# Optimization experiments

Hardware: AMD Instinct MI355X
Metric: run time of the kernel (lower is better)

## Reference

```python
import jax, jax.numpy as jnp
import numpy as np

B, N = 256, 20000

def setup_inputs() -> dict:
    key = jax.random.key(0)
    k1, k2 = jax.random.split(key)
    x_in = jax.random.normal(k1, (B, 1, N, 4), dtype=jnp.float32)
    weights = jax.random.uniform(k2, (B, N), dtype=jnp.float32)
    return {"x_in": x_in, "weights": weights}

def reference(x_in, weights):
    # weighted_8points: x_in [B,1,N,4] -> e_hat [B,9]
    b, _, n, _ = x_in.shape
    xx = x_in[:, 0, :, :]                      # [B,N,4] = (x1, y1, x2, y2)
    x1, y1, x2, y2 = xx[..., 0], xx[..., 1], xx[..., 2], xx[..., 3]
    ones = jnp.ones_like(x1)
    # Epipolar design matrix rows: [x2*x1, x2*y1, x2, y2*x1, y2*y1, y2, x1, y1, 1]
    X = jnp.stack([x2 * x1, x2 * y1, x2,
                   y2 * x1, y2 * y1, y2,
                   x1, y1, ones], axis=-1)      # [B,N,9]
    wX = weights[:, :, None] * X                # [B,N,9]
    XwX = jnp.einsum('bni,bnj->bij', X, wX)     # [B,9,9] symmetric
    # batch_symeig: eigenvectors ascending by eigenvalue; smallest -> column 0
    _, v = jnp.linalg.eigh(XwX)                 # [B,9,9]
    e_hat = v[:, :, 0]                          # [B,9]
    e_hat = e_hat / jnp.linalg.norm(e_hat, axis=1, keepdims=True)
    return e_hat
```

## Files before the change

### kernel.cpp

```cpp
#include <hip/hip_runtime.h>
#include <math.h>

#define BATCH 256
#define NPTS  20000
#define NCHUNK 4
#define PERCH (NPTS / NCHUNK)

__global__ __launch_bounds__(256) void gram_kernel(
    const float4* __restrict__ x, const float* __restrict__ w,
    double* __restrict__ partial)
{
    int b = blockIdx.x;
    int chunk = blockIdx.y;
    int tid = threadIdx.x;

    float acc[45];
#pragma unroll
    for (int k = 0; k < 45; ++k) acc[k] = 0.0f;

    const float4* xb = x + (size_t)b * NPTS;
    const float*  wb = w + (size_t)b * NPTS;
    int base = chunk * PERCH;
    for (int n = base + tid; n < base + PERCH; n += 256) {
        float4 v = xb[n];
        float wt = wb[n];
        float X[9];
        X[0] = v.z * v.x; X[1] = v.z * v.y; X[2] = v.z;
        X[3] = v.w * v.x; X[4] = v.w * v.y; X[5] = v.w;
        X[6] = v.x;       X[7] = v.y;       X[8] = 1.0f;
        int idx = 0;
#pragma unroll
        for (int j = 0; j < 9; ++j) {
            float wXj = wt * X[j];
#pragma unroll
            for (int i = j; i < 9; ++i) {
                acc[idx] += X[i] * wXj;
                ++idx;
            }
        }
    }

#pragma unroll
    for (int k = 0; k < 45; ++k) {
        float v = acc[k];
        for (int off = 32; off > 0; off >>= 1)
            v += __shfl_down(v, off, 64);
        acc[k] = v;
    }
    __shared__ float red[4][45];
    int lane = tid & 63, wv = tid >> 6;
    if (lane == 0) {
#pragma unroll
        for (int k = 0; k < 45; ++k) red[wv][k] = acc[k];
    }
    __syncthreads();
    if (tid < 45) {
        double s = (double)red[0][tid] + (double)red[1][tid]
                 + (double)red[2][tid] + (double)red[3][tid];
        partial[((size_t)b * NCHUNK + chunk) * 45 + tid] = s;
    }
}


__device__ __forceinline__ float f_sign(float a, float b) {
    return (b >= 0.0f) ? fabsf(a) : -fabsf(a);
}

__device__ __forceinline__ float slapy2(float xx, float yy) {
    float xa = fabsf(xx), ya = fabsf(yy);
    float w_ = fmaxf(xa, ya), z_ = fminf(xa, ya);
    if (z_ == 0.0f) return w_;
    float t = z_ / w_;
    return w_ * sqrtf(1.0f + t * t);
}

__device__ __forceinline__ void slartg(float f, float g, float* cs, float* sn, float* r) {
    if (g == 0.0f) { *cs = 1.0f; *sn = 0.0f; *r = f; }
    else if (f == 0.0f) { *cs = 0.0f; *sn = (g >= 0.0f) ? 1.0f : -1.0f; *r = fabsf(g); }
    else {
        float dd = sqrtf(f * f + g * g);
        *cs = fabsf(f) / dd;
        *r  = f_sign(dd, f);
        *sn = g / (*r);
    }
}

__device__ void slaev2(float a, float b, float c_, float* rt1, float* rt2,
                       float* cs1, float* sn1) {
    float sm = a + c_;
    float df = a - c_;
    float adf = fabsf(df);
    float tb = b + b;
    float ab = fabsf(tb);
    float acmx, acmn;
    if (fabsf(a) > fabsf(c_)) { acmx = a; acmn = c_; } else { acmx = c_; acmn = a; }
    float rt;
    if (adf > ab)      { float t = ab / adf; rt = adf * sqrtf(1.0f + t * t); }
    else if (adf < ab) { float t = adf / ab; rt = ab * sqrtf(1.0f + t * t); }
    else               { rt = ab * sqrtf(2.0f); }
    int sgn1;
    if (sm < 0.0f) {
        *rt1 = 0.5f * (sm - rt); sgn1 = -1;
        *rt2 = (acmx / (*rt1)) * acmn - (b / (*rt1)) * b;
    } else if (sm > 0.0f) {
        *rt1 = 0.5f * (sm + rt); sgn1 = 1;
        *rt2 = (acmx / (*rt1)) * acmn - (b / (*rt1)) * b;
    } else {
        *rt1 = 0.5f * rt; *rt2 = -0.5f * rt; sgn1 = 1;
    }
    float cs; int sgn2;
    if (df >= 0.0f) { cs = df + rt; sgn2 = 1; } else { cs = df - rt; sgn2 = -1; }
    float acs = fabsf(cs);
    if (acs > ab) {
        float ct = -tb / cs;
        *sn1 = 1.0f / sqrtf(1.0f + ct * ct);
        *cs1 = ct * (*sn1);
    } else {
        if (ab == 0.0f) { *cs1 = 1.0f; *sn1 = 0.0f; }
        else {
            float tn = -cs / tb;
            *cs1 = 1.0f / sqrtf(1.0f + tn * tn);
            *sn1 = tn * (*cs1);
        }
    }
    if (sgn1 == sgn2) { float tn = *cs1; *cs1 = -(*sn1); *sn1 = tn; }
}

__global__ __launch_bounds__(64) void eig_kernel(
    const double* __restrict__ partial, float* __restrict__ out)
{
    const int n = 9;
    int b = blockIdx.x;
    int lane = threadIdx.x;

    __shared__ float A[10][10];
    __shared__ float Z[10][10];
    __shared__ float dd[11], ee[11], tau[10], cw[10], sw[10], wv[10], zv[10];

    if (lane < 45) {
        const double* p = partial + (size_t)b * (45 * NCHUNK) + lane;
        double s = ((p[0] + p[45]) + p[90]) + p[135];
        int idx = lane, j = 1;
        while (idx >= 10 - j) { idx -= (10 - j); ++j; }
        int i = j + idx;
        A[i][j] = (float)s;
    }

    for (int e = lane; e < 100; e += 64) {
        int r0 = e / 10, c0 = e % 10;
        Z[r0][c0] = (r0 == c0) ? 1.0f : 0.0f;
    }

    for (int i = 1; i <= n - 1; ++i) {
        float alpha = A[i + 1][i];
        float ssq = 0.0f;
        for (int k = i + 2; k <= n; ++k) ssq += A[k][i] * A[k][i];
        float xnorm = sqrtf(ssq);
        float taui;
        if (xnorm == 0.0f) {
            taui = 0.0f;
            if (lane == 0) ee[i] = alpha;
        } else {
            float beta = -f_sign(slapy2(alpha, xnorm), alpha);
            taui = (beta - alpha) / beta;
            float sc = 1.0f / (alpha - beta);
            if (lane < 8 - i) {
                int k = i + 2 + lane;
                A[k][i] *= sc;
            }
            if (lane == 0) ee[i] = beta;
        }
        if (taui != 0.0f) {
            if (lane < 9 - i) {
                int r2 = i + 1 + lane;
                float s2 = 0.0f;
                for (int c2 = i + 1; c2 <= n; ++c2) {
                    float aval = (r2 >= c2) ? A[r2][c2] : A[c2][r2];
                    float vc = (c2 == i + 1) ? 1.0f : A[c2][i];
                    s2 += aval * vc;
                }
                wv[r2] = taui * s2;
            }
            float dot = 0.0f;
            for (int k = i + 1; k <= n; ++k) {
                float vk = (k == i + 1) ? 1.0f : A[k][i];
                dot += wv[k] * vk;
            }
            float alpha2 = -0.5f * taui * dot;
            if (lane < 9 - i) {
                int k = i + 1 + lane;
                float vk = (k == i + 1) ? 1.0f : A[k][i];
                wv[k] += alpha2 * vk;
            }
            int kk = 9 - i;
            int cnt = kk * (kk + 1) / 2;
            if (lane < cnt) {
                int idx = lane, cc = 0;
                while (idx >= kk - cc) { idx -= (kk - cc); ++cc; }
                int c2 = i + 1 + cc;
                int r2 = c2 + idx;
                float vr = (r2 == i + 1) ? 1.0f : A[r2][i];
                float vc = (c2 == i + 1) ? 1.0f : A[c2][i];
                A[r2][c2] -= vr * wv[c2] + wv[r2] * vc;
            }
        }
        if (lane == 0) { dd[i] = A[i][i]; tau[i] = taui; }
    }
    if (lane == 0) dd[n] = A[n][n];

    const float eps    = 5.9604645e-8f;
    const float eps2   = eps * eps;
    const float safmin = 1.17549435e-38f;
    const float safmax = 1.0f / 1.17549435e-38f;
    const float ssfmax = sqrtf(safmax) / 3.0f;
    const float ssfmin = sqrtf(safmin) / eps2;

    int nmaxit = n * 30, jtot = 0;
    int l1 = 1, nm1 = n - 1;
    int l, m, lsv, lend, lendsv, iscale;
    float anorm, p, g, r, c, s, f, btmp, rt1, rt2, tst, mul;

L10:
    if (l1 > n) goto L160;
    if (l1 > 1) { if (lane == 0) ee[l1 - 1] = 0.0f; }
    if (l1 <= nm1) {
        for (m = l1; m <= nm1; ++m) {
            tst = fabsf(ee[m]);
            if (tst == 0.0f) goto L30;
            if (tst <= (sqrtf(fabsf(dd[m])) * sqrtf(fabsf(dd[m + 1]))) * eps) {
                if (lane == 0) ee[m] = 0.0f;
                goto L30;
            }
        }
    }
    m = n;
L30:
    l = l1; lsv = l; lend = m; lendsv = lend; l1 = m + 1;
    if (lend == l) goto L10;

    anorm = 0.0f;
    for (int k = l; k <= lend; ++k) anorm = fmaxf(anorm, fabsf(dd[k]));
    for (int k = l; k <= lend - 1; ++k) anorm = fmaxf(anorm, fabsf(ee[k]));
    iscale = 0;
    if (anorm == 0.0f) goto L10;
    if (anorm > ssfmax) {
        iscale = 1; mul = ssfmax / anorm;
        if (lane <= lend - l) dd[l + lane] *= mul;
        if (lane <  lend - l) ee[l + lane] *= mul;
    } else if (anorm < ssfmin) {
        iscale = 2; mul = ssfmin / anorm;
        if (lane <= lend - l) dd[l + lane] *= mul;
        if (lane <  lend - l) ee[l + lane] *= mul;
    }

    if (fabsf(dd[lend]) < fabsf(dd[l])) { lend = lsv; l = lendsv; }

    if (lend > l) {
L40:
        if (l != lend) {
            for (m = l; m <= lend - 1; ++m) {
                tst = fabsf(ee[m]); tst = tst * tst;
                if (tst <= (eps2 * fabsf(dd[m])) * fabsf(dd[m + 1]) + safmin) goto L60;
            }
        }
        m = lend;
L60:
        if (m < lend) { if (lane == 0) ee[m] = 0.0f; }
        p = dd[l];
        if (m == l) goto L80;
        if (m == l + 1) {
            slaev2(dd[l], ee[l], dd[l + 1], &rt1, &rt2, &c, &s);
            if (lane < 9) {
                int row = lane + 1;
                float temp = Z[row][l + 1];
                Z[row][l + 1] = c * temp - s * Z[row][l];
                Z[row][l]     = s * temp + c * Z[row][l];
            }
            if (lane == 0) { dd[l] = rt1; dd[l + 1] = rt2; ee[l] = 0.0f; }
            l += 2;
            if (l <= lend) goto L40;
            goto L140;
        }
        if (jtot == nmaxit) goto L140;
        ++jtot;
        g = (dd[l + 1] - p) / (2.0f * ee[l]);
        r = slapy2(g, 1.0f);
        g = dd[m] - p + ee[l] / (g + f_sign(r, g));
        s = 1.0f; c = 1.0f; p = 0.0f;
        for (int i = m - 1; i >= l; --i) {
            f = s * ee[i]; btmp = c * ee[i];
            slartg(g, f, &c, &s, &r);
            if (i != m - 1) { if (lane == 0) ee[i + 1] = r; }
            g = dd[i + 1] - p;
            r = (dd[i] - g) * s + 2.0f * c * btmp;
            p = s * r;
            if (lane == 0) dd[i + 1] = g + p;
            g = c * r - btmp;
            if (lane == 0) { cw[i] = c; sw[i] = -s; }
        }
        for (int j = m - 1; j >= l; --j) {
            float ct = cw[j], st = sw[j];
            if (ct != 1.0f || st != 0.0f) {
                if (lane < 9) {
                    int row = lane + 1;
                    float temp = Z[row][j + 1];
                    Z[row][j + 1] = ct * temp - st * Z[row][j];
                    Z[row][j]     = st * temp + ct * Z[row][j];
                }
            }
        }
        if (lane == 0) { dd[l] -= p; ee[l] = g; }
        goto L40;
L80:
        if (lane == 0) dd[l] = p;
        l = l + 1;
        if (l <= lend) goto L40;
        goto L140;
    } else {
L90:
        if (l != lend) {
            for (m = l; m >= lend + 1; --m) {
                tst = fabsf(ee[m - 1]); tst = tst * tst;
                if (tst <= (eps2 * fabsf(dd[m])) * fabsf(dd[m - 1]) + safmin) goto L110;
            }
        }
        m = lend;
L110:
        if (m > lend) { if (lane == 0) ee[m - 1] = 0.0f; }
        p = dd[l];
        if (m == l) goto L130;
        if (m == l - 1) {
            slaev2(dd[l - 1], ee[l - 1], dd[l], &rt1, &rt2, &c, &s);
            if (lane < 9) {
                int row = lane + 1;
                float temp = Z[row][l];
                Z[row][l]     = c * temp - s * Z[row][l - 1];
                Z[row][l - 1] = s * temp + c * Z[row][l - 1];
            }
            if (lane == 0) { dd[l - 1] = rt1; dd[l] = rt2; ee[l - 1] = 0.0f; }
            l -= 2;
            if (l >= lend) goto L90;
            goto L140;
        }
        if (jtot == nmaxit) goto L140;
        ++jtot;
        g = (dd[l - 1] - p) / (2.0f * ee[l - 1]);
        r = slapy2(g, 1.0f);
        g = dd[m] - p + ee[l - 1] / (g + f_sign(r, g));
        s = 1.0f; c = 1.0f; p = 0.0f;
        for (int i = m; i <= l - 1; ++i) {
            f = s * ee[i]; btmp = c * ee[i];
            slartg(g, f, &c, &s, &r);
            if (i != m) { if (lane == 0) ee[i - 1] = r; }
            g = dd[i] - p;
            r = (dd[i + 1] - g) * s + 2.0f * c * btmp;
            p = s * r;
            if (lane == 0) dd[i] = g + p;
            g = c * r - btmp;
            if (lane == 0) { cw[i] = c; sw[i] = s; }
        }
        for (int j = m; j <= l - 1; ++j) {
            float ct = cw[j], st = sw[j];
            if (ct != 1.0f || st != 0.0f) {
                if (lane < 9) {
                    int row = lane + 1;
                    float temp = Z[row][j + 1];
                    Z[row][j + 1] = ct * temp - st * Z[row][j];
                    Z[row][j]     = st * temp + ct * Z[row][j];
                }
            }
        }
        if (lane == 0) { dd[l] -= p; ee[l - 1] = g; }
        goto L90;
L130:
        if (lane == 0) dd[l] = p;
        l = l - 1;
        if (l >= lend) goto L90;
        goto L140;
    }

L140:
    if (iscale == 1) {
        mul = anorm / ssfmax;
        if (lane <= lendsv - lsv) dd[lsv + lane] *= mul;
        if (lane <  lendsv - lsv) ee[lsv + lane] *= mul;
    } else if (iscale == 2) {
        mul = anorm / ssfmin;
        if (lane <= lendsv - lsv) dd[lsv + lane] *= mul;
        if (lane <  lendsv - lsv) ee[lsv + lane] *= mul;
    }
    if (jtot < nmaxit) goto L10;
    goto L160;

L160:
    for (int ii = 2; ii <= n; ++ii) {
        int i = ii - 1, k = i;
        p = dd[i];
        for (int j = ii; j <= n; ++j)
            if (dd[j] < p) { k = j; p = dd[j]; }
        if (k != i) {
            if (lane == 0) { dd[k] = dd[i]; dd[i] = p; }
            if (lane < 9) {
                int row = lane + 1;
                float t = Z[row][i]; Z[row][i] = Z[row][k]; Z[row][k] = t;
            }
        }
    }

    if (lane < 9) zv[lane + 1] = Z[lane + 1][1];
    for (int i2 = n - 1; i2 >= 1; --i2) {
        float ti = tau[i2];
        if (ti != 0.0f) {
            float dotp = zv[i2 + 1];
            for (int k = i2 + 2; k <= n; ++k) dotp += A[k][i2] * zv[k];
            float t = ti * dotp;
            if (lane < 9 - i2) {
                int k = i2 + 1 + lane;
                float upd = (k == i2 + 1) ? t : t * A[k][i2];
                zv[k] -= upd;
            }
        }
    }
    {
        float nrm = 0.0f;
        for (int row = 1; row <= n; ++row) nrm += zv[row] * zv[row];
        nrm = sqrtf(nrm);
        if (lane < 9) out[(size_t)b * 9 + lane] = zv[lane + 1] / nrm;
    }
}

extern "C" void kernel_launch(void* const* d_in, const int* in_sizes, int n_in,
                              void* d_out, int out_size, void* d_ws, size_t ws_size,
                              hipStream_t stream) {
    const float4* x = (const float4*)d_in[0];
    const float*  w = (const float*)d_in[1];
    float* out = (float*)d_out;
    double* partial = (double*)d_ws;

    gram_kernel<<<dim3(BATCH, NCHUNK), dim3(256), 0, stream>>>(x, w, partial);
    eig_kernel<<<dim3(BATCH), dim3(64), 0, stream>>>(partial, out);
}
```

Measured before the change: 206.3 us.

## Keep tridiagonal QL state in registers with readlane broadcasts in eig kernel

Moves the diagonal, off-diagonal and Givens rotation arrays of the implicit QL/QR iteration from shared memory into per-lane registers, read through readlane broadcasts. The eigenvector matrix Z is also held in per-lane register rows and updated with fully unrolled rotation sweeps, then spilled to shared memory only for the final sort. This is meant to remove shared-memory round trips and lane-0 serialized stores in the latency-bound single-wave eigen solver. The cost is more registers and the possibility that readlane with a non-uniform index needs extra handling.

```diff
diff --git a/kernel.cpp b/kernel.cpp
--- a/kernel.cpp
+++ b/kernel.cpp
@@ -74,13 +74,17 @@
     return w_ * sqrtf(1.0f + t * t);
 }
 
+__device__ __forceinline__ float rdl(float v, int i) {
+    return __int_as_float(__builtin_amdgcn_readlane(__float_as_int(v), i));
+}
+
 __device__ __forceinline__ void slartg(float f, float g, float* cs, float* sn, float* r) {
     if (g == 0.0f) { *cs = 1.0f; *sn = 0.0f; *r = f; }
     else if (f == 0.0f) { *cs = 0.0f; *sn = (g >= 0.0f) ? 1.0f : -1.0f; *r = fabsf(g); }
     else {
-        float dd = sqrtf(f * f + g * g);
-        *cs = fabsf(f) / dd;
-        *r  = f_sign(dd, f);
+        float dd2 = sqrtf(f * f + g * g);
+        *cs = fabsf(f) / dd2;
+        *r  = f_sign(dd2, f);
         *sn = g / (*r);
     }
 }
@@ -126,6 +130,24 @@
     if (sgn1 == sgn2) { float tn = *cs1; *cs1 = -(*sn1); *sn1 = tn; }
 }
 
+#define APPLY_QL() do { \
+    _Pragma("unroll") \
+    for (int jz = 8; jz >= 1; --jz) { \
+        float cj = rdl(r_cw, jz), sj = rdl(r_sw, jz); \
+        float tmpz = zz[jz + 1]; \
+        zz[jz + 1] = cj * tmpz - sj * zz[jz]; \
+        zz[jz]     = sj * tmpz + cj * zz[jz]; \
+    } } while (0)
+
+#define APPLY_QR() do { \
+    _Pragma("unroll") \
+    for (int jz = 1; jz <= 8; ++jz) { \
+        float cj = rdl(r_cw, jz), sj = rdl(r_sw, jz); \
+        float tmpz = zz[jz + 1]; \
+        zz[jz + 1] = cj * tmpz - sj * zz[jz]; \
+        zz[jz]     = sj * tmpz + cj * zz[jz]; \
+    } } while (0)
+
 __global__ __launch_bounds__(64) void eig_kernel(
     const double* __restrict__ partial, float* __restrict__ out)
 {
@@ -134,8 +156,11 @@
     int lane = threadIdx.x;
 
     __shared__ float A[10][10];
-    __shared__ float Z[10][10];
-    __shared__ float dd[11], ee[11], tau[10], cw[10], sw[10], wv[10], zv[10];
+    __shared__ float Zl[10][10];
+    __shared__ float ddl[11], eel[11], tau[10], wv[10], zv[10];
+
+    float zz[10];
+    float r_dd, r_ee, r_cw, r_sw;
 
     if (lane < 45) {
         const double* p = partial + (size_t)b * (45 * NCHUNK) + lane;
@@ -144,11 +169,6 @@
         while (idx >= 10 - j) { idx -= (10 - j); ++j; }
         int i = j + idx;
         A[i][j] = (float)s;
-    }
-
-    for (int e = lane; e < 100; e += 64) {
-        int r0 = e / 10, c0 = e % 10;
-        Z[r0][c0] = (r0 == c0) ? 1.0f : 0.0f;
     }
 
     for (int i = 1; i <= n - 1; ++i) {
@@ -159,7 +179,7 @@
         float taui;
         if (xnorm == 0.0f) {
             taui = 0.0f;
-            if (lane == 0) ee[i] = alpha;
+            if (lane == 0) eel[i] = alpha;
         } else {
             float beta = -f_sign(slapy2(alpha, xnorm), alpha);
             taui = (beta - alpha) / beta;
@@ -168,7 +188,7 @@
                 int k = i + 2 + lane;
                 A[k][i] *= sc;
             }
-            if (lane == 0) ee[i] = beta;
+            if (lane == 0) eel[i] = beta;
         }
         if (taui != 0.0f) {
             if (lane < 9 - i) {
@@ -204,9 +224,16 @@
                 A[r2][c2] -= vr * wv[c2] + wv[r2] * vc;
             }
         }
-        if (lane == 0) { dd[i] = A[i][i]; tau[i] = taui; }
-    }
-    if (lane == 0) dd[n] = A[n][n];
+        if (lane == 0) { ddl[i] = A[i][i]; tau[i] = taui; }
+    }
+    if (lane == 0) ddl[n] = A[n][n];
+
+    r_dd = 0.0f; r_ee = 0.0f;
+    if (lane >= 1 && lane <= 9) r_dd = ddl[lane];
+    if (lane >= 1 && lane <= 8) r_ee = eel[lane];
+
+#pragma unroll
+    for (int c0 = 1; c0 <= 9; ++c0) zz[c0] = (lane == c0) ? 1.0f : 0.0f;
 
     const float eps    = 5.9604645e-8f;
     const float eps2   = eps * eps;
@@ -222,13 +249,13 @@
 
 L10:
     if (l1 > n) goto L160;
-    if (l1 > 1) { if (lane == 0) ee[l1 - 1] = 0.0f; }
+    if (l1 > 1) r_ee = (lane == l1 - 1) ? 0.0f : r_ee;
     if (l1 <= nm1) {
         for (m = l1; m <= nm1; ++m) {
-            tst = fabsf(ee[m]);
+            tst = fabsf(rdl(r_ee, m));
             if (tst == 0.0f) goto L30;
-            if (tst <= (sqrtf(fabsf(dd[m])) * sqrtf(fabsf(dd[m + 1]))) * eps) {
-                if (lane == 0) ee[m] = 0.0f;
+            if (tst <= (sqrtf(fabsf(rdl(r_dd, m))) * sqrtf(fabsf(rdl(r_dd, m + 1)))) * eps) {
+                r_ee = (lane == m) ? 0.0f : r_ee;
                 goto L30;
             }
         }
@@ -239,80 +266,73 @@
     if (lend == l) goto L10;
 
     anorm = 0.0f;
-    for (int k = l; k <= lend; ++k) anorm = fmaxf(anorm, fabsf(dd[k]));
-    for (int k = l; k <= lend - 1; ++k) anorm = fmaxf(anorm, fabsf(ee[k]));
+    for (int k = l; k <= lend; ++k) anorm = fmaxf(anorm, fabsf(rdl(r_dd, k)));
+    for (int k = l; k <= lend - 1; ++k) anorm = fmaxf(anorm, fabsf(rdl(r_ee, k)));
     iscale = 0;
     if (anorm == 0.0f) goto L10;
     if (anorm > ssfmax) {
         iscale = 1; mul = ssfmax / anorm;
-        if (lane <= lend - l) dd[l + lane] *= mul;
-        if (lane <  lend - l) ee[l + lane] *= mul;
+        r_dd = (lane >= l && lane <= lend)     ? r_dd * mul : r_dd;
+        r_ee = (lane >= l && lane <= lend - 1) ? r_ee * mul : r_ee;
     } else if (anorm < ssfmin) {
         iscale = 2; mul = ssfmin / anorm;
-        if (lane <= lend - l) dd[l + lane] *= mul;
-        if (lane <  lend - l) ee[l + lane] *= mul;
-    }
-
-    if (fabsf(dd[lend]) < fabsf(dd[l])) { lend = lsv; l = lendsv; }
+        r_dd = (lane >= l && lane <= lend)     ? r_dd * mul : r_dd;
+        r_ee = (lane >= l && lane <= lend - 1) ? r_ee * mul : r_ee;
+    }
+
+    if (fabsf(rdl(r_dd, lend)) < fabsf(rdl(r_dd, l))) { lend = lsv; l = lendsv; }
 
     if (lend > l) {
 L40:
         if (l != lend) {
             for (m = l; m <= lend - 1; ++m) {
-                tst = fabsf(ee[m]); tst = tst * tst;
-                if (tst <= (eps2 * fabsf(dd[m])) * fabsf(dd[m + 1]) + safmin) goto L60;
+                tst = fabsf(rdl(r_ee, m)); tst = tst * tst;
+                if (tst <= (eps2 * fabsf(rdl(r_dd, m))) * fabsf(rdl(r_dd, m + 1)) + safmin) goto L60;
             }
         }
         m = lend;
 L60:
-        if (m < lend) { if (lane == 0) ee[m] = 0.0f; }
-        p = dd[l];
+        if (m < lend) r_ee = (lane == m) ? 0.0f : r_ee;
+        p = rdl(r_dd, l);
         if (m == l) goto L80;
         if (m == l + 1) {
-            slaev2(dd[l], ee[l], dd[l + 1], &rt1, &rt2, &c, &s);
-            if (lane < 9) {
-                int row = lane + 1;
-                float temp = Z[row][l + 1];
-                Z[row][l + 1] = c * temp - s * Z[row][l];
-                Z[row][l]     = s * temp + c * Z[row][l];
-            }
-            if (lane == 0) { dd[l] = rt1; dd[l + 1] = rt2; ee[l] = 0.0f; }
+            slaev2(rdl(r_dd, l), rdl(r_ee, l), rdl(r_dd, l + 1), &rt1, &rt2, &c, &s);
+            r_cw = 1.0f; r_sw = 0.0f;
+            r_cw = (lane == l) ? c : r_cw;
+            r_sw = (lane == l) ? s : r_sw;
+            APPLY_QL();
+            r_dd = (lane == l) ? rt1 : ((lane == l + 1) ? rt2 : r_dd);
+            r_ee = (lane == l) ? 0.0f : r_ee;
             l += 2;
             if (l <= lend) goto L40;
             goto L140;
         }
         if (jtot == nmaxit) goto L140;
         ++jtot;
-        g = (dd[l + 1] - p) / (2.0f * ee[l]);
+        g = (rdl(r_dd, l + 1) - p) / (2.0f * rdl(r_ee, l));
         r = slapy2(g, 1.0f);
-        g = dd[m] - p + ee[l] / (g + f_sign(r, g));
+        g = rdl(r_dd, m) - p + rdl(r_ee, l) / (g + f_sign(r, g));
         s = 1.0f; c = 1.0f; p = 0.0f;
+        r_cw = 1.0f; r_sw = 0.0f;
         for (int i = m - 1; i >= l; --i) {
-            f = s * ee[i]; btmp = c * ee[i];
+            float ei = rdl(r_ee, i);
+            f = s * ei; btmp = c * ei;
             slartg(g, f, &c, &s, &r);
-            if (i != m - 1) { if (lane == 0) ee[i + 1] = r; }
-            g = dd[i + 1] - p;
-            r = (dd[i] - g) * s + 2.0f * c * btmp;
+            if (i != m - 1) r_ee = (lane == i + 1) ? r : r_ee;
+            g = rdl(r_dd, i + 1) - p;
+            r = (rdl(r_dd, i) - g) * s + 2.0f * c * btmp;
             p = s * r;
-            if (lane == 0) dd[i + 1] = g + p;
+            r_dd = (lane == i + 1) ? (g + p) : r_dd;
             g = c * r - btmp;
-            if (lane == 0) { cw[i] = c; sw[i] = -s; }
-        }
-        for (int j = m - 1; j >= l; --j) {
-            float ct = cw[j], st = sw[j];
-            if (ct != 1.0f || st != 0.0f) {
-                if (lane < 9) {
-                    int row = lane + 1;
-                    float temp = Z[row][j + 1];
-                    Z[row][j + 1] = ct * temp - st * Z[row][j];
-                    Z[row][j]     = st * temp + ct * Z[row][j];
-                }
-            }
-        }
-        if (lane == 0) { dd[l] -= p; ee[l] = g; }
+            r_cw = (lane == i) ? c : r_cw;
+            r_sw = (lane == i) ? (-s) : r_sw;
+        }
+        APPLY_QL();
+        r_dd = (lane == l) ? (r_dd - p) : r_dd;
+        r_ee = (lane == l) ? g : r_ee;
         goto L40;
 L80:
-        if (lane == 0) dd[l] = p;
+        r_dd = (lane == l) ? p : r_dd;
         l = l + 1;
         if (l <= lend) goto L40;
         goto L140;
@@ -320,60 +340,53 @@
 L90:
         if (l != lend) {
             for (m = l; m >= lend + 1; --m) {
-                tst = fabsf(ee[m - 1]); tst = tst * tst;
-                if (tst <= (eps2 * fabsf(dd[m])) * fabsf(dd[m - 1]) + safmin) goto L110;
+                tst = fabsf(rdl(r_ee, m - 1)); tst = tst * tst;
+                if (tst <= (eps2 * fabsf(rdl(r_dd, m))) * fabsf(rdl(r_dd, m - 1)) + safmin) goto L110;
             }
         }
         m = lend;
 L110:
-        if (m > lend) { if (lane == 0) ee[m - 1] = 0.0f; }
-        p = dd[l];
+        if (m > lend) r_ee = (lane == m - 1) ? 0.0f : r_ee;
+        p = rdl(r_dd, l);
         if (m == l) goto L130;
         if (m == l - 1) {
-            slaev2(dd[l - 1], ee[l - 1], dd[l], &rt1, &rt2, &c, &s);
-            if (lane < 9) {
-                int row = lane + 1;
-                float temp = Z[row][l];
-                Z[row][l]     = c * temp - s * Z[row][l - 1];
-                Z[row][l - 1] = s * temp + c * Z[row][l - 1];
-            }
-            if (lane == 0) { dd[l - 1] = rt1; dd[l] = rt2; ee[l - 1] = 0.0f; }
+            slaev2(rdl(r_dd, l - 1), rdl(r_ee, l - 1), rdl(r_dd, l), &rt1, &rt2, &c, &s);
+            r_cw = 1.0f; r_sw = 0.0f;
+            r_cw = (lane == l - 1) ? c : r_cw;
+            r_sw = (lane == l - 1) ? s : r_sw;
+            APPLY_QR();
+            r_dd = (lane == l - 1) ? rt1 : ((lane == l) ? rt2 : r_dd);
+            r_ee = (lane == l - 1) ? 0.0f : r_ee;
             l -= 2;
             if (l >= lend) goto L90;
             goto L140;
         }
         if (jtot == nmaxit) goto L140;
         ++jtot;
-        g = (dd[l - 1] - p) / (2.0f * ee[l - 1]);
+        g = (rdl(r_dd, l - 1) - p) / (2.0f * rdl(r_ee, l - 1));
         r = slapy2(g, 1.0f);
-        g = dd[m] - p + ee[l - 1] / (g + f_sign(r, g));
+        g = rdl(r_dd, m) - p + rdl(r_ee, l - 1) / (g + f_sign(r, g));
         s = 1.0f; c = 1.0f; p = 0.0f;
+        r_cw = 1.0f; r_sw = 0.0f;
         for (int i = m; i <= l - 1; ++i) {
-            f = s * ee[i]; btmp = c * ee[i];
+            float ei = rdl(r_ee, i);
+            f = s * ei; btmp = c * ei;
             slartg(g, f, &c, &s, &r);
-            if (i != m) { if (lane == 0) ee[i - 1] = r; }
-            g = dd[i] - p;
-            r = (dd[i + 1] - g) * s + 2.0f * c * btmp;
+            if (i != m) r_ee = (lane == i - 1) ? r : r_ee;
+            g = rdl(r_dd, i) - p;
+            r = (rdl(r_dd, i + 1) - g) * s + 2.0f * c * btmp;
             p = s * r;
-            if (lane == 0) dd[i] = g + p;
+            r_dd = (lane == i) ? (g + p) : r_dd;
             g = c * r - btmp;
-            if (lane == 0) { cw[i] = c; sw[i] = s; }
-        }
-        for (int j = m; j <= l - 1; ++j) {
-            float ct = cw[j], st = sw[j];
-            if (ct != 1.0f || st != 0.0f) {
-                if (lane < 9) {
-                    int row = lane + 1;
-                    float temp = Z[row][j + 1];
-                    Z[row][j + 1] = ct * temp - st * Z[row][j];
-                    Z[row][j]     = st * temp + ct * Z[row][j];
-                }
-            }
-        }
-        if (lane == 0) { dd[l] -= p; ee[l - 1] = g; }
+            r_cw = (lane == i) ? c : r_cw;
+            r_sw = (lane == i) ? s : r_sw;
+        }
+        APPLY_QR();
+        r_dd = (lane == l) ? (r_dd - p) : r_dd;
+        r_ee = (lane == l - 1) ? g : r_ee;
         goto L90;
 L130:
-        if (lane == 0) dd[l] = p;
+        r_dd = (lane == l) ? p : r_dd;
         l = l - 1;
         if (l >= lend) goto L90;
         goto L140;
@@ -382,32 +395,40 @@
 L140:
     if (iscale == 1) {
         mul = anorm / ssfmax;
-        if (lane <= lendsv - lsv) dd[lsv + lane] *= mul;
-        if (lane <  lendsv - lsv) ee[lsv + lane] *= mul;
+        r_dd = (lane >= lsv && lane <= lendsv)     ? r_dd * mul : r_dd;
+        r_ee = (lane >= lsv && lane <= lendsv - 1) ? r_ee * mul : r_ee;
     } else if (iscale == 2) {
         mul = anorm / ssfmin;
-        if (lane <= lendsv - lsv) dd[lsv + lane] *= mul;
-        if (lane <  lendsv - lsv) ee[lsv + lane] *= mul;
+        r_dd = (lane >= lsv && lane <= lendsv)     ? r_dd * mul : r_dd;
+        r_ee = (lane >= lsv && lane <= lendsv - 1) ? r_ee * mul : r_ee;
     }
     if (jtot < nmaxit) goto L10;
     goto L160;
 
 L160:
+    if (lane >= 1 && lane <= 9) {
+#pragma unroll
+        for (int c0 = 1; c0 <= 9; ++c0) Zl[lane][c0] = zz[c0];
+    }
+
     for (int ii = 2; ii <= n; ++ii) {
         int i = ii - 1, k = i;
-        p = dd[i];
-        for (int j = ii; j <= n; ++j)
-            if (dd[j] < p) { k = j; p = dd[j]; }
+        p = rdl(r_dd, i);
+        for (int j = ii; j <= n; ++j) {
+            float dj = rdl(r_dd, j);
+            if (dj < p) { k = j; p = dj; }
+        }
         if (k != i) {
-            if (lane == 0) { dd[k] = dd[i]; dd[i] = p; }
-            if (lane < 9) {
-                int row = lane + 1;
-                float t = Z[row][i]; Z[row][i] = Z[row][k]; Z[row][k] = t;
-            }
-        }
-    }
-
-    if (lane < 9) zv[lane + 1] = Z[lane + 1][1];
+            float di = rdl(r_dd, i);
+            r_dd = (lane == k) ? di : r_dd;
+            r_dd = (lane == i) ? p  : r_dd;
+            if (lane >= 1 && lane <= 9) {
+                float t = Zl[lane][i]; Zl[lane][i] = Zl[lane][k]; Zl[lane][k] = t;
+            }
+        }
+    }
+
+    if (lane < 9) zv[lane + 1] = Zl[lane + 1][1];
     for (int i2 = n - 1; i2 >= 1; --i2) {
         float ti = tau[i2];
         if (ti != 0.0f) {
```

Result: faster. 193.2 us (-6.3%).
